# Kernel optimization log

Measured on AMD Instinct MI355X. Metric: run time of the kernel, lower is better.

The kernel has to match this reference:

```python
import jax, jax.numpy as jnp
import numpy as np

V, T, E, H, L = 32000, 1024, 1024, 16, 6
D = E // H
FF = 4 * E
B = 2


def _ln(x, s, b, eps=1e-5):
    m = x.mean(-1, keepdims=True)
    v = x.var(-1, keepdims=True)
    return (x - m) * jax.lax.rsqrt(v + eps) * s + b


def setup_inputs() -> dict:
    key = jax.random.key(0)
    ks = jax.random.split(key, 16)
    std = 0.02
    inp = {
        "idx": jax.random.randint(ks[0], (B, T), 0, V),
        "tok_w": jax.random.normal(ks[1], (V, E)) * std,
        "pos_emb": jax.random.normal(ks[2], (1, T, E)) * std,
        # stacked per-layer params [L, ...]
        "ln1_s": jnp.ones((L, E)), "ln1_b": jnp.zeros((L, E)),
        "wq": jax.random.normal(ks[3], (L, E, E)) * std,
        "wk": jax.random.normal(ks[4], (L, E, E)) * std,
        "wv": jax.random.normal(ks[5], (L, E, E)) * std,
        "wo": jax.random.normal(ks[6], (L, E, E)) * std,
        "bo": jnp.zeros((L, E)),
        "ln2_s": jnp.ones((L, E)), "ln2_b": jnp.zeros((L, E)),
        "w1": jax.random.normal(ks[7], (L, E, FF)) * std,
        "b1": jnp.zeros((L, FF)),
        "w2": jax.random.normal(ks[8], (L, FF, E)) * std,
        "b2": jnp.zeros((L, E)),
        "lnf_s": jnp.ones((E,)), "lnf_b": jnp.zeros((E,)),
        "head_w": jax.random.normal(ks[9], (E, V)) * std,
        "head_b": jnp.zeros((V,)),
    }
    return inp


def _gpt(idx, tok_w, pos_emb, ln1_s, ln1_b, wq, wk, wv, wo, bo,
         ln2_s, ln2_b, w1, b1, w2, b2, lnf_s, lnf_b, head_w, head_b):
    x = tok_w[idx] + pos_emb[0, :T]                      # [B,T,E]
    mask = jnp.tril(jnp.ones((T, T), dtype=bool))        # causal mask
    scale = 1.0 / np.sqrt(D)

    def step(x, p):
        l1s, l1b, q_w, k_w, v_w, o_w, o_b, l2s, l2b, f1, fb1, f2, fb2 = p
        h = _ln(x, l1s, l1b)
        q = (h @ q_w).reshape(B, T, H, D)
        k = (h @ k_w).reshape(B, T, H, D)
        v = (h @ v_w).reshape(B, T, H, D)
        att = jnp.einsum('bthd,bshd->bhts', q, k) * scale  # [B,H,T,T]
        att = jnp.where(mask, att, -jnp.inf)
        att = jax.nn.softmax(att, axis=-1)
        o = jnp.einsum('bhts,bshd->bthd', att, v).reshape(B, T, E)
        x = x + o @ o_w + o_b
        h2 = _ln(x, l2s, l2b)
        x = x + jax.nn.relu(h2 @ f1 + fb1) @ f2 + fb2
        return x, None

    params = (ln1_s, ln1_b, wq, wk, wv, wo, bo, ln2_s, ln2_b, w1, b1, w2, b2)
    x, _ = jax.lax.scan(step, x, params)
    x = _ln(x, lnf_s, lnf_b)
    return x @ head_w + head_b                           # logits [B,T,V]


def reference(idx, tok_w, pos_emb, ln1_s, ln1_b, wq, wk, wv, wo, bo,
              ln2_s, ln2_b, w1, b1, w2, b2, lnf_s, lnf_b, head_w, head_b):
    return _gpt(idx, tok_w, pos_emb, ln1_s, ln1_b, wq, wk, wv, wo, bo,
                ln2_s, ln2_b, w1, b1, w2, b2, lnf_s, lnf_b, head_w, head_b)
```

## Files before the change

kernel.cpp:

```cpp
#include <hip/hip_runtime.h>


#define T_SEQ 1024
#define E_DIM 1024
#define H_NUM 16
#define D_HEAD 64
#define L_NUM 6
#define FF_DIM 4096
#define B_NUM 2
#define M_ROWS 2048

using bf16x8 = __attribute__((ext_vector_type(8))) __bf16;
using f32x4  = __attribute__((ext_vector_type(4))) float;

__device__ __forceinline__ unsigned short f2bf(float f) {
  unsigned int u = __float_as_uint(f);
  u += 0x7fffu + ((u >> 16) & 1u);
  return (unsigned short)(u >> 16);
}

__device__ __forceinline__ void gload_lds16(const void* g, void* l) {
  __builtin_amdgcn_global_load_lds(
      (const __attribute__((address_space(1))) unsigned int*)g,
      (__attribute__((address_space(3))) unsigned int*)l, 16, 0, 0);
}

__global__ __launch_bounds__(256) void embed_k(const int* __restrict__ idx,
                                               const float* __restrict__ tok_w,
                                               const float* __restrict__ pos,
                                               float* __restrict__ x) {
  const int i = blockIdx.x;
  const int t = i & (T_SEQ - 1);
  const int tok = idx[i];
  const float4 a = ((const float4*)(tok_w + (size_t)tok * E_DIM))[threadIdx.x];
  const float4 p = ((const float4*)(pos + (size_t)t * E_DIM))[threadIdx.x];
  float4 o;
  o.x = a.x + p.x; o.y = a.y + p.y; o.z = a.z + p.z; o.w = a.w + p.w;
  ((float4*)(x + (size_t)i * E_DIM))[threadIdx.x] = o;
}

__device__ __forceinline__ void ln_body(const float* __restrict__ x,
                                        const float* __restrict__ s,
                                        const float* __restrict__ b,
                                        unsigned short* __restrict__ out,
                                        int blk) {
  const int wave = threadIdx.x >> 6, lane = threadIdx.x & 63;
  const int row = blk * 4 + wave;
  const float4* xr = (const float4*)(x + (size_t)row * E_DIM);
  float4 v[4];
  float sum = 0.f, sq = 0.f;
  #pragma unroll
  for (int i = 0; i < 4; ++i) {
    v[i] = xr[lane + 64 * i];
    sum += v[i].x + v[i].y + v[i].z + v[i].w;
    sq  += v[i].x * v[i].x + v[i].y * v[i].y + v[i].z * v[i].z + v[i].w * v[i].w;
  }
  #pragma unroll
  for (int off = 1; off < 64; off <<= 1) {
    sum += __shfl_xor(sum, off);
    sq  += __shfl_xor(sq, off);
  }
  const float mean = sum * (1.0f / E_DIM);
  const float var  = sq * (1.0f / E_DIM) - mean * mean;
  const float inv  = 1.0f / sqrtf(var + 1e-5f);
  unsigned short* orow = out + (size_t)row * E_DIM;
  #pragma unroll
  for (int i = 0; i < 4; ++i) {
    const float4 sv = ((const float4*)s)[lane + 64 * i];
    const float4 bv = ((const float4*)b)[lane + 64 * i];
    ushort4 o;
    o.x = f2bf((v[i].x - mean) * inv * sv.x + bv.x);
    o.y = f2bf((v[i].y - mean) * inv * sv.y + bv.y);
    o.z = f2bf((v[i].z - mean) * inv * sv.z + bv.z);
    o.w = f2bf((v[i].w - mean) * inv * sv.w + bv.w);
    *(ushort4*)(orow + 4 * (lane + 64 * i)) = o;
  }
}

__global__ __launch_bounds__(256) void ln_k(const float* __restrict__ x,
                                            const float* __restrict__ s,
                                            const float* __restrict__ b,
                                            unsigned short* __restrict__ out) {
  ln_body(x, s, b, out, blockIdx.x);
}

__device__ __forceinline__ void trans_body(const float* __restrict__ W,
                                           unsigned short* __restrict__ WT,
                                           int K, int N, int b,
                                           float (*tile)[33]) {
  const int nbn = N >> 5;
  const int n0 = (b % nbn) << 5, k0 = (b / nbn) << 5;
  const int tx = threadIdx.x & 31, ty = threadIdx.x >> 5;
  #pragma unroll
  for (int i = ty; i < 32; i += 8)
    tile[i][tx] = W[(size_t)(k0 + i) * N + n0 + tx];
  __syncthreads();
  #pragma unroll
  for (int i = ty; i < 32; i += 8)
    WT[(size_t)(n0 + i) * K + k0 + tx] = f2bf(tile[tx][i]);
}

__global__ __launch_bounds__(256) void ln_trans_k(
    const float* __restrict__ x, const float* __restrict__ s,
    const float* __restrict__ b, unsigned short* __restrict__ outh,
    const float* __restrict__ wq, const float* __restrict__ wk,
    const float* __restrict__ wv, const float* __restrict__ wo,
    const float* __restrict__ w1, const float* __restrict__ w2,
    unsigned short* __restrict__ wt_qkv, unsigned short* __restrict__ wt_o,
    unsigned short* __restrict__ wt_f1, unsigned short* __restrict__ wt_f2) {
  __shared__ float tile[32][33];
  const int bid = blockIdx.x;
  if (bid < 512) { ln_body(x, s, b, outh, bid); return; }
  const int tb = bid - 512;
  if (tb < 3072) {
    const int w = tb >> 10;
    const float* W = (w == 0) ? wq : (w == 1) ? wk : wv;
    trans_body(W, wt_qkv + (size_t)w * 1024 * 1024, 1024, 1024, tb & 1023, tile);
  } else if (tb < 4096) {
    trans_body(wo, wt_o, 1024, 1024, tb - 3072, tile);
  } else if (tb < 8192) {
    trans_body(w1, wt_f1, 1024, 4096, tb - 4096, tile);
  } else {
    trans_body(w2, wt_f2, 4096, 1024, tb - 8192, tile);
  }
}

__global__ __launch_bounds__(256) void lnf_trans_k(
    const float* __restrict__ x, const float* __restrict__ s,
    const float* __restrict__ b, unsigned short* __restrict__ outh,
    const float* __restrict__ head_w, unsigned short* __restrict__ wth) {
  __shared__ float tile[32][33];
  const int bid = blockIdx.x;
  if (bid < 512) { ln_body(x, s, b, outh, bid); return; }
  trans_body(head_w, wth, 1024, 32000, bid - 512, tile);
}

template<int BM, bool RELU, bool BIAS, bool RES, bool OBF16>
__global__ __launch_bounds__(256) void gemm_k(const unsigned short* __restrict__ A,
                                              const unsigned short* __restrict__ WT,
                                              const float* __restrict__ bias,
                                              const float* __restrict__ res,
                                              void* __restrict__ Cout,
                                              int ldc, int K) {
  constexpr int BN = 128;
  constexpr int BK = 64;
  constexpr int MF = BM / 32;
  constexpr int AJ = (BM * BK * 2 / 1024) / 4;
  constexpr int BJ = (BN * BK * 2 / 1024) / 4;
  __shared__ __align__(16) unsigned short As[2][BM][BK];
  __shared__ __align__(16) unsigned short Bs[2][BN][BK];
  const int tid = threadIdx.x;
  const int row0 = blockIdx.x * BM, col0 = blockIdx.y * BN;
  const int wave = tid >> 6, lane = tid & 63;
  const int wm = (wave >> 1) * (BM / 2), wn = (wave & 1) * 64;
  const int lr = lane & 15, lg = lane >> 4;
  const int ric = lane >> 3, sslot = lane & 7;

  auto stage = [&](int buf, int k0) {
    #pragma unroll
    for (int j = 0; j < AJ; ++j) {
      const int c = wave + 4 * j;
      const int row = c * 8 + ric;
      const int sp = sslot ^ (row & 7);
      gload_lds16(A + (size_t)(row0 + row) * K + k0 + sp * 8,
                  (char*)&As[buf][0][0] + c * 1024);
    }
    #pragma unroll
    for (int j = 0; j < BJ; ++j) {
      const int c = wave + 4 * j;
      const int row = c * 8 + ric;
      const int sp = sslot ^ (row & 7);
      gload_lds16(WT + (size_t)(col0 + row) * K + k0 + sp * 8,
                  (char*)&Bs[buf][0][0] + c * 1024);
    }
  };

  f32x4 acc[MF][4] = {};
  const int nt = K / BK;
  stage(0, 0);
  __syncthreads();
  for (int t = 0; t < nt; ++t) {
    const int cur = t & 1;
    if (t + 1 < nt) stage(cur ^ 1, (t + 1) * BK);
    #pragma unroll
    for (int ks = 0; ks < 2; ++ks) {
      bf16x8 af[MF], bfr[4];
      #pragma unroll
      for (int m = 0; m < MF; ++m) {
        const int r = wm + m * 16 + lr;
        const int s = (ks * 4 + lg) ^ (r & 7);
        af[m] = *(const bf16x8*)((const char*)&As[cur][0][0] + r * 128 + s * 16);
      }
      #pragma unroll
      for (int n = 0; n < 4; ++n) {
        const int r = wn + n * 16 + lr;
        const int s = (ks * 4 + lg) ^ (r & 7);
        bfr[n] = *(const bf16x8*)((const char*)&Bs[cur][0][0] + r * 128 + s * 16);
      }
      #pragma unroll
      for (int m = 0; m < MF; ++m)
        #pragma unroll
        for (int n = 0; n < 4; ++n)
          acc[m][n] = __builtin_amdgcn_mfma_f32_16x16x32_bf16(af[m], bfr[n], acc[m][n], 0, 0, 0);
    }
    __syncthreads();
  }
  float* Cf = (float*)Cout;
  unsigned short* Cb = (unsigned short*)Cout;
  #pragma unroll
  for (int m = 0; m < MF; ++m) {
    #pragma unroll
    for (int n = 0; n < 4; ++n) {
      const int col = col0 + wn + (n << 4) + lr;
      const float bv = BIAS ? bias[col] : 0.0f;
      #pragma unroll
      for (int r = 0; r < 4; ++r) {
        const int row = row0 + wm + (m << 4) + (lg << 2) + r;
        float val = acc[m][n][r] + bv;
        if (RELU) val = fmaxf(val, 0.0f);
        if (RES)  val += res[(size_t)row * ldc + col];
        if (OBF16) Cb[(size_t)row * ldc + col] = f2bf(val);
        else       Cf[(size_t)row * ldc + col] = val;
      }
    }
  }
}

#define LOAD_AF(HALF)                                                         \
  _Pragma("unroll")                                                           \
  for (int mf = 0; mf < 4; ++mf) {                                            \
    const int rr = wm * 64 + mf * 16 + lr;                                    \
    _Pragma("unroll")                                                         \
    for (int ks = 0; ks < 2; ++ks)                                            \
      af[mf][ks] = *(const bf16x8*)&As[buf][HALF][rr]                         \
          [(((ks << 2) + lgp) ^ (rr & 7)) << 3];                              \
  }
#define LOAD_BF(HALF)                                                         \
  _Pragma("unroll")                                                           \
  for (int nf = 0; nf < 2; ++nf) {                                            \
    const int rr = wn * 32 + nf * 16 + lr;                                    \
    _Pragma("unroll")                                                         \
    for (int ks = 0; ks < 2; ++ks)                                            \
      bfq[nf][ks] = *(const bf16x8*)&Bs[buf][HALF][rr]                        \
          [(((ks << 2) + lgp) ^ (rr & 7)) << 3];                              \
  }
#define MFMA_Q(MH, NH)                                                        \
  __builtin_amdgcn_s_setprio(1);                                              \
  _Pragma("unroll")                                                           \
  for (int mf = 0; mf < 4; ++mf)                                              \
    _Pragma("unroll")                                                         \
    for (int nf = 0; nf < 2; ++nf) {                                          \
      acc[MH][NH][mf][nf] = __builtin_amdgcn_mfma_f32_16x16x32_bf16(          \
          af[mf][0], bfq[nf][0], acc[MH][NH][mf][nf], 0, 0, 0);               \
      acc[MH][NH][mf][nf] = __builtin_amdgcn_mfma_f32_16x16x32_bf16(          \
          af[mf][1], bfq[nf][1], acc[MH][NH][mf][nf], 0, 0, 0);               \
    }                                                                         \
  __builtin_amdgcn_s_setprio(0);

__global__ __launch_bounds__(512) void gemm8_k(
    const unsigned short* __restrict__ A, const unsigned short* __restrict__ WT,
    const float* __restrict__ bias, float* __restrict__ C,
    int ldc, int K, int mgrid) {
  constexpr int BK = 64;
  __shared__ __align__(16) unsigned short As[2][2][128][64];
  __shared__ __align__(16) unsigned short Bs[2][2][128][64];
  const int tid = threadIdx.x;
  const int wave = tid >> 6, lane = tid & 63;
  const int wm = wave >> 2, wn = wave & 3;
  const int lr = lane & 15, lgp = lane >> 4;
  const int nwg = gridDim.x;
  const int q = nwg >> 3, r = nwg & 7;
  const int xcd = blockIdx.x & 7;
  const int lgid = (xcd < r ? xcd * (q + 1) : r * (q + 1) + (xcd - r) * q)
                   + (blockIdx.x >> 3);
  const int row0 = (lgid % mgrid) * 256, col0 = (lgid / mgrid) * 256;
  const int srow = lane >> 3, sslot = lane & 7;

  auto stA = [&](int buf, int half, int k0) {
    #pragma unroll
    for (int j = 0; j < 2; ++j) {
      const int row = j * 64 + wave * 8 + srow;
      const int sp = sslot ^ (row & 7);
      gload_lds16(A + (size_t)(row0 + half * 128 + row) * K + k0 + sp * 8,
                  (char*)&As[buf][half][0][0] + j * 8192 + wave * 1024);
    }
  };
  auto stB = [&](int buf, int half, int k0) {
    #pragma unroll
    for (int j = 0; j < 2; ++j) {
      const int row = j * 64 + wave * 8 + srow;
      const int sp = sslot ^ (row & 7);
      gload_lds16(WT + (size_t)(col0 + half * 128 + row) * K + k0 + sp * 8,
                  (char*)&Bs[buf][half][0][0] + j * 8192 + wave * 1024);
    }
  };

  f32x4 acc[2][2][4][2] = {};
  bf16x8 af[4][2], bfq[2][2];
  const int nt = K / BK;

  stA(0, 0, 0); stB(0, 1, 0); stB(0, 0, 0); stA(0, 1, 0);
  if (nt > 1) {
    stA(1, 0, BK); stB(1, 1, BK);
    asm volatile("s_waitcnt vmcnt(4)" ::: "memory");
  } else {
    asm volatile("s_waitcnt vmcnt(0)" ::: "memory");
  }
  __builtin_amdgcn_s_barrier();

  for (int t = 0; t < nt; ++t) {
    const int buf = t & 1, nbuf = buf ^ 1;
    const int k0 = t * BK;
    LOAD_AF(0)
    LOAD_BF(0)
    if (t + 1 < nt) { stB(nbuf, 0, k0 + BK); stA(nbuf, 1, k0 + BK); }
    __builtin_amdgcn_s_barrier();
    MFMA_Q(0, 0)
    __builtin_amdgcn_s_barrier();
    LOAD_BF(1)
    __builtin_amdgcn_s_barrier();
    MFMA_Q(0, 1)
    __builtin_amdgcn_s_barrier();
    LOAD_AF(1)
    if (t + 2 < nt) stA(buf, 0, k0 + 2 * BK);
    __builtin_amdgcn_s_barrier();
    MFMA_Q(1, 1)
    __builtin_amdgcn_s_barrier();
    LOAD_BF(0)
    if (t + 2 < nt) stB(buf, 1, k0 + 2 * BK);
    __builtin_amdgcn_s_barrier();
    MFMA_Q(1, 0)
    if (t + 1 < nt) {
      if (t + 2 < nt) asm volatile("s_waitcnt vmcnt(4)" ::: "memory");
      else            asm volatile("s_waitcnt vmcnt(0)" ::: "memory");
    }
    __builtin_amdgcn_s_barrier();
  }

  #pragma unroll
  for (int mh = 0; mh < 2; ++mh)
    #pragma unroll
    for (int nh = 0; nh < 2; ++nh)
      #pragma unroll
      for (int mf = 0; mf < 4; ++mf)
        #pragma unroll
        for (int nf = 0; nf < 2; ++nf) {
          const int col = col0 + nh * 128 + wn * 32 + nf * 16 + lr;
          const float bv = bias[col];
          #pragma unroll
          for (int rr = 0; rr < 4; ++rr) {
            const int row = row0 + mh * 128 + wm * 64 + mf * 16 + lgp * 4 + rr;
            C[(size_t)row * ldc + col] = acc[mh][nh][mf][nf][rr] + bv;
          }
        }
}

#define QBLK 64
#define KBLK 64
__global__ __launch_bounds__(256) void fattn_k(const unsigned short* __restrict__ qkv,
                                               unsigned short* __restrict__ ob) {
  const int qt = (T_SEQ / QBLK - 1) - blockIdx.x;
  const int h = blockIdx.y, b = blockIdx.z;
  const int tid = threadIdx.x;
  const int wave = tid >> 6, lane = tid & 63;
  const int lr = lane & 15, lg = lane >> 4;
  const int q0 = qt * QBLK;

  __shared__ __align__(16) unsigned short Qs[QBLK][72];
  __shared__ __align__(16) unsigned short Ks[KBLK][72];
  __shared__ __align__(16) unsigned short Vt[D_HEAD][72];
  __shared__ __align__(16) unsigned short Ps[QBLK][72];

  const size_t base = (size_t)b * T_SEQ * 3072 + (size_t)h * 64;
  const int srow = tid >> 3, scol = (tid & 7) << 3;

  uint4 kreg[2], vreg[2];
  auto load_kv = [&](int s0) {
    #pragma unroll
    for (int it = 0; it < 2; ++it) {
      const int row = srow + it * 32;
      kreg[it] = *(const uint4*)(qkv + base + 1024 + (size_t)(s0 + row) * 3072 + scol);
      vreg[it] = *(const uint4*)(qkv + base + 2048 + (size_t)(s0 + row) * 3072 + scol);
    }
  };
  auto write_kv = [&]() {
    #pragma unroll
    for (int it = 0; it < 2; ++it) {
      const int row = srow + it * 32;
      *(uint4*)&Ks[row][scol] = kreg[it];
      const unsigned short* ws = (const unsigned short*)&vreg[it];
      #pragma unroll
      for (int j = 0; j < 8; ++j) Vt[scol + j][row] = ws[j];
    }
  };

  #pragma unroll
  for (int it = 0; it < 2; ++it) {
    const int row = srow + it * 32;
    *(uint4*)&Qs[row][scol] =
        *(const uint4*)(qkv + base + (size_t)(q0 + row) * 3072 + scol);
  }
  load_kv(0);
  write_kv();
  __syncthreads();
  bf16x8 qf[2];
  #pragma unroll
  for (int ks = 0; ks < 2; ++ks)
    qf[ks] = *(const bf16x8*)&Qs[wave * 16 + lr][ks * 32 + lg * 8];

  f32x4 acc_o[4] = {};
  float mrow[4], lrow[4];
  #pragma unroll
  for (int r = 0; r < 4; ++r) { mrow[r] = -3.0e38f; lrow[r] = 0.f; }

  const int ntile = qt + 1;
  for (int kt = 0; kt < ntile; ++kt) {
    const int s0 = kt * KBLK;
    f32x4 sacc[4] = {};
    #pragma unroll
    for (int ks = 0; ks < 2; ++ks) {
      #pragma unroll
      for (int nf = 0; nf < 4; ++nf) {
        bf16x8 kf = *(const bf16x8*)&Ks[nf * 16 + lr][ks * 32 + lg * 8];
        sacc[nf] = __builtin_amdgcn_mfma_f32_16x16x32_bf16(qf[ks], kf, sacc[nf], 0, 0, 0);
      }
    }
    if (kt + 1 < ntile) load_kv(s0 + KBLK);
    float sv[4][4];
    #pragma unroll
    for (int nf = 0; nf < 4; ++nf)
      #pragma unroll
      for (int r = 0; r < 4; ++r) sv[nf][r] = sacc[nf][r] * 0.125f;
    if (kt == ntile - 1) {
      #pragma unroll
      for (int nf = 0; nf < 4; ++nf) {
        const int s = s0 + nf * 16 + lr;
        #pragma unroll
        for (int r = 0; r < 4; ++r) {
          const int q = q0 + wave * 16 + lg * 4 + r;
          if (s > q) sv[nf][r] = -3.0e38f;
        }
      }
    }
    float p[4][4];
    #pragma unroll
    for (int r = 0; r < 4; ++r) {
      float mx = fmaxf(fmaxf(sv[0][r], sv[1][r]), fmaxf(sv[2][r], sv[3][r]));
      #pragma unroll
      for (int off = 1; off < 16; off <<= 1) mx = fmaxf(mx, __shfl_xor(mx, off));
      const float mnew = fmaxf(mrow[r], mx);
      const float alpha = __expf(mrow[r] - mnew);
      mrow[r] = mnew;
      float sum = 0.f;
      #pragma unroll
      for (int nf = 0; nf < 4; ++nf) {
        p[nf][r] = __expf(sv[nf][r] - mnew);
        sum += p[nf][r];
      }
      #pragma unroll
      for (int off = 1; off < 16; off <<= 1) sum += __shfl_xor(sum, off);
      lrow[r] = lrow[r] * alpha + sum;
      #pragma unroll
      for (int df = 0; df < 4; ++df) acc_o[df][r] *= alpha;
    }
    #pragma unroll
    for (int nf = 0; nf < 4; ++nf)
      #pragma unroll
      for (int r = 0; r < 4; ++r)
        Ps[wave * 16 + lg * 4 + r][nf * 16 + lr] = f2bf(p[nf][r]);
    #pragma unroll
    for (int ks = 0; ks < 2; ++ks) {
      bf16x8 pa = *(const bf16x8*)&Ps[wave * 16 + lr][ks * 32 + lg * 8];
      #pragma unroll
      for (int df = 0; df < 4; ++df) {
        bf16x8 vf = *(const bf16x8*)&Vt[df * 16 + lr][ks * 32 + lg * 8];
        acc_o[df] = __builtin_amdgcn_mfma_f32_16x16x32_bf16(pa, vf, acc_o[df], 0, 0, 0);
      }
    }
    __syncthreads();
    if (kt + 1 < ntile) {
      write_kv();
      __syncthreads();
    }
  }
  #pragma unroll
  for (int r = 0; r < 4; ++r) {
    const float inv = 1.0f / lrow[r];
    const int row = q0 + wave * 16 + lg * 4 + r;
    #pragma unroll
    for (int df = 0; df < 4; ++df)
      ob[((size_t)b * T_SEQ + row) * E_DIM + h * 64 + df * 16 + lr] =
          f2bf(acc_o[df][r] * inv);
  }
}

extern "C" void kernel_launch(void* const* d_in, const int* in_sizes, int n_in,
                              void* d_out, int out_size, void* d_ws, size_t ws_size,
                              hipStream_t stream) {
  (void)in_sizes; (void)n_in; (void)out_size; (void)ws_size;
  const int*   idx    = (const int*)d_in[0];
  const float* tok_w  = (const float*)d_in[1];
  const float* pos    = (const float*)d_in[2];
  const float* ln1_s  = (const float*)d_in[3];
  const float* ln1_b  = (const float*)d_in[4];
  const float* wq     = (const float*)d_in[5];
  const float* wk     = (const float*)d_in[6];
  const float* wv     = (const float*)d_in[7];
  const float* wo     = (const float*)d_in[8];
  const float* bo     = (const float*)d_in[9];
  const float* ln2_s  = (const float*)d_in[10];
  const float* ln2_b  = (const float*)d_in[11];
  const float* w1     = (const float*)d_in[12];
  const float* b1     = (const float*)d_in[13];
  const float* w2     = (const float*)d_in[14];
  const float* b2     = (const float*)d_in[15];
  const float* lnf_s  = (const float*)d_in[16];
  const float* lnf_b  = (const float*)d_in[17];
  const float* head_w = (const float*)d_in[18];
  const float* head_b = (const float*)d_in[19];
  float* out = (float*)d_out;

  char* p = (char*)d_ws;
  float* x            = (float*)p;          p += (size_t)M_ROWS * E_DIM * 4;
  unsigned short* qkvb= (unsigned short*)p; p += (size_t)M_ROWS * 3072 * 2;
  unsigned short* h   = (unsigned short*)p; p += (size_t)M_ROWS * E_DIM * 2;
  unsigned short* obuf= (unsigned short*)p; p += (size_t)M_ROWS * E_DIM * 2;
  unsigned short* ff  = (unsigned short*)p; p += (size_t)M_ROWS * FF_DIM * 2;
  unsigned short* wt  = (unsigned short*)p; p += (size_t)3072 * E_DIM * 2;
  unsigned short* wto = (unsigned short*)p; p += (size_t)E_DIM * E_DIM * 2;
  unsigned short* wtf1= (unsigned short*)p; p += (size_t)FF_DIM * E_DIM * 2;
  unsigned short* wtf2= (unsigned short*)p; p += (size_t)E_DIM * FF_DIM * 2;
  unsigned short* wth = (unsigned short*)p; p += (size_t)32000 * E_DIM * 2;

  embed_k<<<M_ROWS, 256, 0, stream>>>(idx, tok_w, pos, x);

  for (int l = 0; l < L_NUM; ++l) {
    const size_t lEE = (size_t)l * E_DIM * E_DIM;
    const size_t lEF = (size_t)l * E_DIM * FF_DIM;
    ln_trans_k<<<12800, 256, 0, stream>>>(
        x, ln1_s + l * E_DIM, ln1_b + l * E_DIM, h,
        wq + lEE, wk + lEE, wv + lEE, wo + lEE, w1 + lEF, w2 + lEF,
        wt, wto, wtf1, wtf2);
    gemm_k<64,false,false,false,true><<<dim3(32, 24), 256, 0, stream>>>(
        h, wt, nullptr, nullptr, qkvb, 3072, E_DIM);
    fattn_k<<<dim3(T_SEQ / QBLK, H_NUM, B_NUM), 256, 0, stream>>>(qkvb, obuf);
    gemm_k<32,false,true,true,false><<<dim3(64, 8), 256, 0, stream>>>(
        obuf, wto, bo + l * E_DIM, x, x, E_DIM, E_DIM);
    ln_k<<<M_ROWS / 4, 256, 0, stream>>>(x, ln2_s + l * E_DIM, ln2_b + l * E_DIM, h);
    gemm_k<64,true,true,false,true><<<dim3(32, 32), 256, 0, stream>>>(
        h, wtf1, b1 + l * FF_DIM, nullptr, ff, FF_DIM, E_DIM);
    gemm_k<32,false,true,true,false><<<dim3(64, 8), 256, 0, stream>>>(
        ff, wtf2, b2 + l * E_DIM, x, x, E_DIM, FF_DIM);
  }

  lnf_trans_k<<<32512, 256, 0, stream>>>(x, lnf_s, lnf_b, h, head_w, wth);
  gemm8_k<<<1000, 512, 0, stream>>>(h, wth, head_b, out, 32000, E_DIM, 8);
}
```

Measured before the change: 1.360 ms.

## Double-buffer B fragments in head GEMM and widen attention query tile to 128

The LM-head GEMM now holds two B-fragment register sets, so the second B half stays in registers and the redundant LDS reload of B half 0 before the last MFMA quarter is dropped. The attention kernel moves from 64 to 128 query rows per block with 512 threads (8 waves). Each K/V tile loaded into LDS is therefore reused by twice as many query rows. The causal mask is now applied to any KV tile that crosses the block's first query row. The trade-offs are more VGPR pressure in the GEMM and half as many attention blocks, with more causal load imbalance between them.

```diff
diff --git a/kernel.cpp b/kernel.cpp
--- a/kernel.cpp
+++ b/kernel.cpp
@@ -235,25 +235,25 @@
       af[mf][ks] = *(const bf16x8*)&As[buf][HALF][rr]                         \
           [(((ks << 2) + lgp) ^ (rr & 7)) << 3];                              \
   }
-#define LOAD_BF(HALF)                                                         \
+#define LOAD_BF(HALF, DST)                                                    \
   _Pragma("unroll")                                                           \
   for (int nf = 0; nf < 2; ++nf) {                                            \
     const int rr = wn * 32 + nf * 16 + lr;                                    \
     _Pragma("unroll")                                                         \
     for (int ks = 0; ks < 2; ++ks)                                            \
-      bfq[nf][ks] = *(const bf16x8*)&Bs[buf][HALF][rr]                        \
+      DST[nf][ks] = *(const bf16x8*)&Bs[buf][HALF][rr]                        \
           [(((ks << 2) + lgp) ^ (rr & 7)) << 3];                              \
   }
-#define MFMA_Q(MH, NH)                                                        \
+#define MFMA_Q(MH, NH, BQ)                                                    \
   __builtin_amdgcn_s_setprio(1);                                              \
   _Pragma("unroll")                                                           \
   for (int mf = 0; mf < 4; ++mf)                                              \
     _Pragma("unroll")                                                         \
     for (int nf = 0; nf < 2; ++nf) {                                          \
       acc[MH][NH][mf][nf] = __builtin_amdgcn_mfma_f32_16x16x32_bf16(          \
-          af[mf][0], bfq[nf][0], acc[MH][NH][mf][nf], 0, 0, 0);               \
+          af[mf][0], BQ[nf][0], acc[MH][NH][mf][nf], 0, 0, 0);                \
       acc[MH][NH][mf][nf] = __builtin_amdgcn_mfma_f32_16x16x32_bf16(          \
-          af[mf][1], bfq[nf][1], acc[MH][NH][mf][nf], 0, 0, 0);               \
+          af[mf][1], BQ[nf][1], acc[MH][NH][mf][nf], 0, 0, 0);                \
     }                                                                         \
   __builtin_amdgcn_s_setprio(0);
 
@@ -296,7 +296,7 @@
   };
 
   f32x4 acc[2][2][4][2] = {};
-  bf16x8 af[4][2], bfq[2][2];
+  bf16x8 af[4][2], bfq0[2][2], bfq1[2][2];
   const int nt = K / BK;
 
   stA(0, 0, 0); stB(0, 1, 0); stB(0, 0, 0); stA(0, 1, 0);
@@ -312,24 +312,23 @@
     const int buf = t & 1, nbuf = buf ^ 1;
     const int k0 = t * BK;
     LOAD_AF(0)
-    LOAD_BF(0)
+    LOAD_BF(0, bfq0)
     if (t + 1 < nt) { stB(nbuf, 0, k0 + BK); stA(nbuf, 1, k0 + BK); }
     __builtin_amdgcn_s_barrier();
-    MFMA_Q(0, 0)
-    __builtin_amdgcn_s_barrier();
-    LOAD_BF(1)
-    __builtin_amdgcn_s_barrier();
-    MFMA_Q(0, 1)
+    MFMA_Q(0, 0, bfq0)
+    __builtin_amdgcn_s_barrier();
+    LOAD_BF(1, bfq1)
+    __builtin_amdgcn_s_barrier();
+    MFMA_Q(0, 1, bfq1)
     __builtin_amdgcn_s_barrier();
     LOAD_AF(1)
     if (t + 2 < nt) stA(buf, 0, k0 + 2 * BK);
     __builtin_amdgcn_s_barrier();
-    MFMA_Q(1, 1)
-    __builtin_amdgcn_s_barrier();
-    LOAD_BF(0)
+    MFMA_Q(1, 1, bfq1)
+    __builtin_amdgcn_s_barrier();
     if (t + 2 < nt) stB(buf, 1, k0 + 2 * BK);
     __builtin_amdgcn_s_barrier();
-    MFMA_Q(1, 0)
+    MFMA_Q(1, 0, bfq0)
     if (t + 1 < nt) {
       if (t + 2 < nt) asm volatile("s_waitcnt vmcnt(4)" ::: "memory");
       else            asm volatile("s_waitcnt vmcnt(0)" ::: "memory");
@@ -355,9 +354,9 @@
         }
 }
 
-#define QBLK 64
+#define QBLK 128
 #define KBLK 64
-__global__ __launch_bounds__(256) void fattn_k(const unsigned short* __restrict__ qkv,
+__global__ __launch_bounds__(512) void fattn_k(const unsigned short* __restrict__ qkv,
                                                unsigned short* __restrict__ ob) {
   const int qt = (T_SEQ / QBLK - 1) - blockIdx.x;
   const int h = blockIdx.y, b = blockIdx.z;
@@ -374,29 +373,21 @@
   const size_t base = (size_t)b * T_SEQ * 3072 + (size_t)h * 64;
   const int srow = tid >> 3, scol = (tid & 7) << 3;
 
-  uint4 kreg[2], vreg[2];
+  uint4 kreg, vreg;
   auto load_kv = [&](int s0) {
-    #pragma unroll
-    for (int it = 0; it < 2; ++it) {
-      const int row = srow + it * 32;
-      kreg[it] = *(const uint4*)(qkv + base + 1024 + (size_t)(s0 + row) * 3072 + scol);
-      vreg[it] = *(const uint4*)(qkv + base + 2048 + (size_t)(s0 + row) * 3072 + scol);
-    }
+    kreg = *(const uint4*)(qkv + base + 1024 + (size_t)(s0 + srow) * 3072 + scol);
+    vreg = *(const uint4*)(qkv + base + 2048 + (size_t)(s0 + srow) * 3072 + scol);
   };
   auto write_kv = [&]() {
-    #pragma unroll
-    for (int it = 0; it < 2; ++it) {
-      const int row = srow + it * 32;
-      *(uint4*)&Ks[row][scol] = kreg[it];
-      const unsigned short* ws = (const unsigned short*)&vreg[it];
-      #pragma unroll
-      for (int j = 0; j < 8; ++j) Vt[scol + j][row] = ws[j];
-    }
+    *(uint4*)&Ks[srow][scol] = kreg;
+    const unsigned short* ws = (const unsigned short*)&vreg;
+    #pragma unroll
+    for (int j = 0; j < 8; ++j) Vt[scol + j][srow] = ws[j];
   };
 
   #pragma unroll
   for (int it = 0; it < 2; ++it) {
-    const int row = srow + it * 32;
+    const int row = srow + it * 64;
     *(uint4*)&Qs[row][scol] =
         *(const uint4*)(qkv + base + (size_t)(q0 + row) * 3072 + scol);
   }
@@ -413,7 +404,7 @@
   #pragma unroll
   for (int r = 0; r < 4; ++r) { mrow[r] = -3.0e38f; lrow[r] = 0.f; }
 
-  const int ntile = qt + 1;
+  const int ntile = 2 * (qt + 1);
   for (int kt = 0; kt < ntile; ++kt) {
     const int s0 = kt * KBLK;
     f32x4 sacc[4] = {};
@@ -431,14 +422,14 @@
     for (int nf = 0; nf < 4; ++nf)
       #pragma unroll
       for (int r = 0; r < 4; ++r) sv[nf][r] = sacc[nf][r] * 0.125f;
-    if (kt == ntile - 1) {
+    if (s0 + KBLK - 1 > q0) {
       #pragma unroll
       for (int nf = 0; nf < 4; ++nf) {
         const int s = s0 + nf * 16 + lr;
         #pragma unroll
         for (int r = 0; r < 4; ++r) {
-          const int q = q0 + wave * 16 + lg * 4 + r;
-          if (s > q) sv[nf][r] = -3.0e38f;
+          const int qq = q0 + wave * 16 + lg * 4 + r;
+          if (s > qq) sv[nf][r] = -3.0e38f;
         }
       }
     }
@@ -543,7 +534,7 @@
         wt, wto, wtf1, wtf2);
     gemm_k<64,false,false,false,true><<<dim3(32, 24), 256, 0, stream>>>(
         h, wt, nullptr, nullptr, qkvb, 3072, E_DIM);
-    fattn_k<<<dim3(T_SEQ / QBLK, H_NUM, B_NUM), 256, 0, stream>>>(qkvb, obuf);
+    fattn_k<<<dim3(T_SEQ / QBLK, H_NUM, B_NUM), 512, 0, stream>>>(qkvb, obuf);
     gemm_k<32,false,true,true,false><<<dim3(64, 8), 256, 0, stream>>>(
         obuf, wto, bo + l * E_DIM, x, x, E_DIM, E_DIM);
     ln_k<<<M_ROWS / 4, 256, 0, stream>>>(x, ln2_s + l * E_DIM, ln2_b + l * E_DIM, h);
```

Measured after the change: 1.320 ms. -2.9%, faster.
